# Optimization experiments

Measured on AMD Instinct MI355X. Metric: run time of the kernel, lower is better.

Reference implementation:

```python
import math
import jax, jax.numpy as jnp
import numpy as np
from jax.scipy.special import erf

D = 128                # cubic box / image size (even)
B, T = 4, 2            # particles, candidate poses per particle
GRID_DIST_DEGS = 8.0
GRID_STEP_DEGS = 2.0
PIXEL_SIZE = 1.5       # Angstrom / px
MAX_SHIFT_FRACTION = 0.2
TOP_K = 2
HALF_PARTICLE = 0.5 * D


def _rot_z(a):
    c, s = jnp.cos(a), jnp.sin(a)
    z, o = jnp.zeros_like(a), jnp.ones_like(a)
    return jnp.stack([jnp.stack([c, -s, z], -1),
                      jnp.stack([s, c, z], -1),
                      jnp.stack([z, z, o], -1)], -2)


def _rot_y(a):
    c, s = jnp.cos(a), jnp.sin(a)
    z, o = jnp.zeros_like(a), jnp.ones_like(a)
    return jnp.stack([jnp.stack([c, z, s], -1),
                      jnp.stack([z, o, z], -1),
                      jnp.stack([-s, z, c], -1)], -2)


def _euler_zyz_to_matrix(ang):
    # RELION convention ZYZ: R = Rz(a) @ Ry(b) @ Rz(c)
    return _rot_z(ang[..., 0]) @ _rot_y(ang[..., 1]) @ _rot_z(ang[..., 2])


def _so3_grid_rotmats():
    n = math.ceil(GRID_DIST_DEGS / GRID_STEP_DEGS)
    n = n if n % 2 == 1 else n + 1
    half = GRID_DIST_DEGS / 2.0
    a = np.linspace(-half, half, n)
    g = np.stack(np.meshgrid(a, a, a, indexing='ij'), -1).reshape(-1, 3)
    return _euler_zyz_to_matrix(jnp.deg2rad(jnp.asarray(g, jnp.float32)))


def _compute_dft(vol):
    # sinc^2 gridding pre-filter, then fftshifted rfftn of fftshifted volume
    d = vol.shape[-1]
    f = jnp.fft.fftshift(jnp.fft.fftfreq(d)).astype(vol.dtype)
    fz, fy, fx = jnp.meshgrid(f, f, f, indexing='ij')
    r = jnp.sqrt(fz * fz + fy * fy + fx * fx)
    vol = vol * jnp.sinc(r) ** 2
    dft = jnp.fft.rfftn(jnp.fft.fftshift(vol, axes=(-3, -2, -1)), axes=(-3, -2, -1))
    return jnp.fft.fftshift(dft, axes=(-3, -2))


def _trilinear_complex(vol, z, y, x):
    # trilinear interpolation into a complex 3D array, zero outside bounds
    Dz, Dy, Dx = vol.shape
    z0f, y0f, x0f = jnp.floor(z), jnp.floor(y), jnp.floor(x)
    fz, fy, fx = z - z0f, y - y0f, x - x0f
    z0, y0, x0 = z0f.astype(jnp.int32), y0f.astype(jnp.int32), x0f.astype(jnp.int32)

    def corner(zi, yi, xi, w):
        valid = (zi >= 0) & (zi < Dz) & (yi >= 0) & (yi < Dy) & (xi >= 0) & (xi < Dx)
        v = vol[jnp.clip(zi, 0, Dz - 1), jnp.clip(yi, 0, Dy - 1), jnp.clip(xi, 0, Dx - 1)]
        return jnp.where(valid, v * w, jnp.zeros((), vol.dtype))

    out = corner(z0, y0, x0, (1 - fz) * (1 - fy) * (1 - fx))
    out = out + corner(z0, y0, x0 + 1, (1 - fz) * (1 - fy) * fx)
    out = out + corner(z0, y0 + 1, x0, (1 - fz) * fy * (1 - fx))
    out = out + corner(z0, y0 + 1, x0 + 1, (1 - fz) * fy * fx)
    out = out + corner(z0 + 1, y0, x0, fz * (1 - fy) * (1 - fx))
    out = out + corner(z0 + 1, y0, x0 + 1, fz * (1 - fy) * fx)
    out = out + corner(z0 + 1, y0 + 1, x0, fz * fy * (1 - fx))
    out = out + corner(z0 + 1, y0 + 1, x0 + 1, fz * fy * fx)
    return out


def _extract_central_slices_rfft_3d(vol_rfft, d, rotmats):
    # rotated central-slice extraction from a fftshifted rfft 3D volume
    fy = jnp.fft.fftshift(jnp.fft.fftfreq(d)).astype(jnp.float32)
    fx = jnp.fft.rfftfreq(d).astype(jnp.float32)
    gy, gx = jnp.meshgrid(fy, fx, indexing='ij')            # (H, Wr)
    coords = jnp.stack([jnp.zeros_like(gy), gy, gx], -1)    # zyx, z=0 plane
    Rzyx = rotmats[..., ::-1, ::-1]                         # xyz rotmat -> zyx
    rot = jnp.einsum('...ij,hwj->...hwi', Rzyx, coords)     # (...,H,Wr,3)
    conj_mask = rot[..., 2] < 0                             # redundant half
    rot = jnp.where(conj_mask[..., None], -rot, rot)
    zi = rot[..., 0] * d + d // 2
    yi = rot[..., 1] * d + d // 2
    xi = rot[..., 2] * d
    s = _trilinear_complex(vol_rfft, zi, yi, xi)
    return jnp.where(conj_mask, jnp.conj(s), s)


def _forward(vol, imgs, ctf, rotmats, grid_rotmats):
    d = vol.shape[-1]
    vol_rfft = _compute_dft(vol)                            # (d, d, d//2+1)
    # _real_to_fourier
    fimg = jnp.fft.fftshift(
        jnp.fft.rfftn(jnp.fft.fftshift(imgs, axes=(-2, -1)), axes=(-2, -1)),
        axes=(-2,))                                         # (B, d, d//2+1)
    # compose pose candidates with the local SO3 grid: rotmats @ grid_rotmats
    exp_R = jnp.einsum('gjk,btij->btgik', grid_rotmats, rotmats)   # (B,T,G,3,3)
    projs = _extract_central_slices_rfft_3d(vol_rfft, d, exp_R)    # (B,T,G,H,Wr)
    projs = projs * ctf[:, None, None]
    # correlate_dft_2d
    prod = fimg[:, None, None] * jnp.conj(projs)
    prod = jnp.fft.ifftshift(prod, axes=(-2,))
    corrs = jnp.fft.ifftshift(jnp.fft.irfftn(prod, s=(d, d), axes=(-2, -1)),
                              axes=(-2, -1))                # (B,T,G,d,d) real
    # constrained peak search within max_shift_fraction window
    delta = math.ceil(d * (1.0 - MAX_SHIFT_FRACTION) / 2)
    h0 = delta
    c = corrs[..., h0:d - delta, h0:d - delta]
    maxJ = jnp.max(c, -1)
    argJ = jnp.argmax(c, -1)
    perImgCorr = jnp.max(maxJ, -1)                          # (B,T,G)
    argI = jnp.argmax(maxJ, -1)
    col = jnp.take_along_axis(argJ, argI[..., None], -1)[..., 0]
    shiftsXY = jnp.stack([h0 + col, h0 + argI], -1)         # (B,T,G,2) as (x,y)
    b = perImgCorr.shape[0]
    nrots = perImgCorr.shape[2]
    flat = perImgCorr.reshape(b, -1)                        # (B, T*G)
    maxCorrs, maxIdxs = jax.lax.top_k(flat, TOP_K)
    bestShifts = jnp.take_along_axis(shiftsXY.reshape(b, -1, 2),
                                     maxIdxs[..., None], axis=1)   # (B,K,2)
    mean = jnp.mean(flat, -1, keepdims=True)
    std = jnp.std(flat, -1, keepdims=True, ddof=1)
    comparedWeight = 0.5 * (1.0 + erf((maxCorrs - mean) / (std * 1.4142135623730951)))
    predShiftsAngs = -(bestShifts.astype(jnp.float32) - HALF_PARTICLE) * PIXEL_SIZE
    predRotMats = grid_rotmats[maxIdxs % nrots]             # (B,K,3,3)
    return maxCorrs, predRotMats, predShiftsAngs, comparedWeight


def setup_inputs() -> dict:
    key = jax.random.key(0)
    kv, ki, kc, kr = jax.random.split(key, 4)
    vol = jax.random.normal(kv, (D, D, D), jnp.float32)
    imgs = jax.random.normal(ki, (B, D, D), jnp.float32)
    ctf = jax.random.uniform(kc, (B, D, D // 2 + 1), jnp.float32, -1.0, 1.0)
    ang = jax.random.uniform(kr, (B, T, 3), jnp.float32, -np.pi, np.pi)
    rotmats = _euler_zyz_to_matrix(ang)
    grid_rotmats = _so3_grid_rotmats()
    return {"vol": vol, "imgs": imgs, "ctf": ctf, "rotmats": rotmats,
            "grid_rotmats": grid_rotmats}


def reference(vol, imgs, ctf, rotmats, grid_rotmats):
    return _forward(vol, imgs, ctf, rotmats, grid_rotmats)
```

## Files before the change

### kernel.cpp

```cpp
#include <hip/hip_runtime.h>
#include <hip/hip_fp16.h>
#include <math.h>
#include <float.h>

#define DD   128
#define KX   65
#define NB   4
#define NTT  2
#define NG   125
#define NBTG (NB*NTT*NG)
#define WIN  24
#define H0   52

#define QZ  132
#define QY  131
#define QX  68
#define QPLANE (QY*QX)
#define QN  (QZ*QY*QX)

typedef unsigned int u32;

__device__ __forceinline__ float2 cmul(float2 a, float2 b){
    return make_float2(a.x*b.x - a.y*b.y, a.x*b.y + a.y*b.x);
}

__device__ __forceinline__ void make_tw(float2* sTw, int tid){
    if (tid < 128){
        float s, c;
        sincosf((float)tid * (float)(M_PI/64.0), &s, &c);
        sTw[tid] = make_float2(c, s);
    }
}

__global__ __launch_bounds__(256) void k_stageA(const float* __restrict__ vol,
                       const float* __restrict__ imgs,
                       float2* __restrict__ A1, float2* __restrict__ B1){
    __shared__ float2 sZ [16*DD];
    __shared__ float2 sZ2[16*DD];
    __shared__ float2 sTw[128];
    int tid = threadIdx.x;
    int bid = blockIdx.x;
    make_tw(sTw, tid);
    __syncthreads();

    if (bid < 512){
        int z = bid >> 2, q = bid & 3;
        int y0 = q*32;
        float fz = (z-64)*(1.0f/128.0f);
        for (int i = tid; i < 16*DD; i += 256){
            int p = i >> 7, x = i & 127;
            int yA = y0 + 2*p;
            float fx = (x-64)*(1.0f/128.0f);
            float fyA = (yA-64)*(1.0f/128.0f);
            float fyB = fyA + (1.0f/128.0f);
            float b2 = fz*fz + fx*fx;
            float rA = sqrtf(b2 + fyA*fyA);
            float rB = sqrtf(b2 + fyB*fyB);
            float sA = (rA > 0.f) ? (sinf((float)M_PI*rA)/((float)M_PI*rA)) : 1.f;
            float sB = (rB > 0.f) ? (sinf((float)M_PI*rB)/((float)M_PI*rB)) : 1.f;
            float a = vol[(z*DD + yA)*DD + x] * sA * sA;
            float b = vol[(z*DD + yA+1)*DD + x] * sB * sB;
            sZ[i] = make_float2(a, b);
        }
        __syncthreads();
        for (int i = tid; i < 16*32; i += 256){
            int p = i >> 5, x1 = i & 31;
            int b0 = p*DD + x1;
            float2 a = sZ[b0], bb = sZ[b0+32], c2 = sZ[b0+64], d = sZ[b0+96];
            float acx=a.x+c2.x, acy=a.y+c2.y;
            float amx=a.x-c2.x, amy=a.y-c2.y;
            float bdx=bb.x+d.x, bdy=bb.y+d.y;
            float bmx=bb.x-d.x, bmy=bb.y-d.y;
            sZ[b0   ] = make_float2(acx+bdx, acy+bdy);
            sZ[b0+32] = make_float2(amx+bmy, amy-bmx);
            sZ[b0+64] = make_float2(acx-bdx, acy-bdy);
            sZ[b0+96] = make_float2(amx-bmy, amy+bmx);
        }
        __syncthreads();
        for (int i = tid; i < 16*32; i += 256){
            int p = i >> 5, r5 = i & 31;
            int c = r5 >> 3, x2 = r5 & 7;
            int b0 = p*DD + 32*c + x2;
            float2 u0 = sZ[b0], u1 = sZ[b0+8], u2 = sZ[b0+16], u3 = sZ[b0+24];
            float2 w1 = sTw[(8*c)&127];  w1.y = -w1.y;
            float2 w2 = sTw[(16*c)&127]; w2.y = -w2.y;
            float2 w3 = sTw[(24*c)&127]; w3.y = -w3.y;
            float2 t1 = cmul(u1,w1), t2 = cmul(u2,w2), t3 = cmul(u3,w3);
            float2 pp = make_float2(u0.x+t2.x, u0.y+t2.y);
            float2 qq = make_float2(u0.x-t2.x, u0.y-t2.y);
            float2 rr = make_float2(t1.x+t3.x, t1.y+t3.y);
            float2 ss = make_float2(t1.x-t3.x, t1.y-t3.y);
            sZ[b0   ] = make_float2(pp.x+rr.x, pp.y+rr.y);
            sZ[b0+8 ] = make_float2(qq.x+ss.y, qq.y-ss.x);
            sZ[b0+16] = make_float2(pp.x-rr.x, pp.y-rr.y);
            sZ[b0+24] = make_float2(qq.x-ss.y, qq.y+ss.x);
        }
        __syncthreads();
        for (int i = tid; i < 16*DD; i += 256){
            int p = i >> 7, k = i & 127;
            int c = k & 3, s = (k >> 2) & 3;
            const float2* v = &sZ[p*DD + 32*c + 8*s];
            float ar0=0,ai0=0,ar1=0,ai1=0;
            int j = 0;
            #pragma unroll
            for (int x2 = 0; x2 < 8; x2 += 2){
                float2 v0 = v[x2], v1 = v[x2+1];
                float2 e0 = sTw[j]; int jn = (j + k)&127;
                float2 e1 = sTw[jn];
                ar0 += v0.x*e0.x + v0.y*e0.y;  ai0 += v0.y*e0.x - v0.x*e0.y;
                ar1 += v1.x*e1.x + v1.y*e1.y;  ai1 += v1.y*e1.x - v1.x*e1.y;
                j = (jn + k)&127;
            }
            sZ2[i] = make_float2(ar0+ar1, ai0+ai1);
        }
        __syncthreads();
        for (int i = tid; i < 16*KX; i += 256){
            int p = i / KX, k = i - p*KX;
            float2 Zk = sZ2[p*DD + k];
            float2 Zm = sZ2[p*DD + ((128-k)&127)];
            float2 A = make_float2(0.5f*(Zk.x+Zm.x), 0.5f*(Zk.y-Zm.y));
            float Dx = Zk.x - Zm.x, Dy = Zk.y + Zm.y;
            float2 Bv = make_float2(0.5f*Dy, -0.5f*Dx);
            int yA = y0 + 2*p;
            A1[(z*DD + yA  )*KX + k] = A;
            A1[(z*DD + yA+1)*KX + k] = Bv;
        }
    } else {
        int o = (bid - 512)*256 + tid;
        if (o >= NB*DD*KX) return;
        int b = o / (DD*KX);
        int r = o - b*DD*KX;
        int y = r / KX, k = r - y*KX;
        const float* row = imgs + (b*DD + y)*DD;
        float ar0=0,ai0=0,ar1=0,ai1=0,ar2=0,ai2=0,ar3=0,ai3=0;
        int i0=0, i1=k&127, i2=(2*k)&127, i3=(3*k)&127;
        int st = (4*k)&127;
        for (int x = 0; x < DD; x += 4){
            float v0=row[x], v1=row[x+1], v2=row[x+2], v3=row[x+3];
            float2 e0=sTw[i0], e1=sTw[i1], e2=sTw[i2], e3=sTw[i3];
            ar0 += v0*e0.x; ai0 -= v0*e0.y;
            ar1 += v1*e1.x; ai1 -= v1*e1.y;
            ar2 += v2*e2.x; ai2 -= v2*e2.y;
            ar3 += v3*e3.x; ai3 -= v3*e3.y;
            i0=(i0+st)&127; i1=(i1+st)&127; i2=(i2+st)&127; i3=(i3+st)&127;
        }
        B1[o] = make_float2(ar0+ar1+ar2+ar3, ai0+ai1+ai2+ai3);
    }
}

__global__ __launch_bounds__(256) void k_stageB(const float2* __restrict__ A1,
                       const float* __restrict__ ctf, const float2* __restrict__ B1,
                       float2* __restrict__ A2, float2* __restrict__ Fc){
    __shared__ float2 sU[32*KX];
    __shared__ float2 sTw[128];
    int tid = threadIdx.x;
    int bid = blockIdx.x;
    make_tw(sTw, tid);
    __syncthreads();

    if (bid < 512){
        int z = bid >> 2, c = bid & 3;
        const float2* base = A1 + z*DD*KX;
        for (int i = tid; i < 32*KX; i += 256){
            int n = i / KX, kk = i - n*KX;
            float2 a  = base[(n    )*KX + kk];
            float2 bb = base[(n+32)*KX + kk];
            float2 c2 = base[(n+64)*KX + kk];
            float2 d  = base[(n+96)*KX + kk];
            float acx = a.x + c2.x, acy = a.y + c2.y;
            float amx = a.x - c2.x, amy = a.y - c2.y;
            float bdx = bb.x + d.x, bdy = bb.y + d.y;
            float bmx = bb.x - d.x, bmy = bb.y - d.y;
            float2 u;
            if (c == 0)      u = make_float2(acx + bdx, acy + bdy);
            else if (c == 2) u = make_float2(acx - bdx, acy - bdy);
            else if (c == 1) u = make_float2(amx + bmy, amy - bmx);
            else             u = make_float2(amx - bmy, amy + bmx);
            sU[i] = u;
        }
        __syncthreads();
        float2 w1 = sTw[(8*c)&127];  w1.y = -w1.y;
        float2 w2 = sTw[(16*c)&127]; w2.y = -w2.y;
        float2 w3 = sTw[(24*c)&127]; w3.y = -w3.y;
        for (int i = tid; i < 8*KX; i += 256){
            int n2 = i / KX, kk = i - n2*KX;
            int b0 = n2*KX + kk;
            float2 u0 = sU[b0], u1 = sU[b0+8*KX], u2 = sU[b0+16*KX], u3 = sU[b0+24*KX];
            float2 t1 = cmul(u1,w1), t2 = cmul(u2,w2), t3 = cmul(u3,w3);
            float2 p = make_float2(u0.x+t2.x, u0.y+t2.y);
            float2 q = make_float2(u0.x-t2.x, u0.y-t2.y);
            float2 r = make_float2(t1.x+t3.x, t1.y+t3.y);
            float2 s = make_float2(t1.x-t3.x, t1.y-t3.y);
            sU[b0       ] = make_float2(p.x+r.x, p.y+r.y);
            sU[b0+ 8*KX ] = make_float2(q.x+s.y, q.y-s.x);
            sU[b0+16*KX ] = make_float2(p.x-r.x, p.y-r.y);
            sU[b0+24*KX ] = make_float2(q.x-s.y, q.y+s.x);
        }
        __syncthreads();
        for (int o = tid; o < 32*KX; o += 256){
            int m = o / KX, kk = o - m*KX;
            int ky = 4*m + c;
            int s4 = m & 3;
            const float2* v = &sU[(8*s4)*KX + kk];
            float ar0=0,ai0=0,ar1=0,ai1=0;
            int j = 0;
            #pragma unroll
            for (int n2 = 0; n2 < 8; n2 += 2){
                float2 v0 = v[n2*KX], v1 = v[(n2+1)*KX];
                float2 e0 = sTw[j]; int jn = (j + ky)&127;
                float2 e1 = sTw[jn];
                ar0 += v0.x*e0.x + v0.y*e0.y;  ai0 += v0.y*e0.x - v0.x*e0.y;
                ar1 += v1.x*e1.x + v1.y*e1.y;  ai1 += v1.y*e1.x - v1.x*e1.y;
                j = (jn + ky)&127;
            }
            A2[(z*DD + ky)*KX + kk] = make_float2(ar0+ar1, ai0+ai1);
        }
    } else {
        int o = (bid - 512)*256 + tid;
        if (o >= NB*DD*KX) return;
        int b = o / (DD*KX);
        int r = o - b*DD*KX;
        int h = r / KX, k = r - h*KX;
        int kky = (h + 64) & 127;
        const float2* col = B1 + b*DD*KX + k;
        float ar0=0,ai0=0,ar1=0,ai1=0,ar2=0,ai2=0,ar3=0,ai3=0;
        int i0=0, i1=kky&127, i2=(2*kky)&127, i3=(3*kky)&127;
        int st = (4*kky)&127;
        for (int y = 0; y < DD; y += 4){
            float2 v0=col[(y+0)*KX], v1=col[(y+1)*KX];
            float2 v2=col[(y+2)*KX], v3=col[(y+3)*KX];
            float2 e0=sTw[i0], e1=sTw[i1], e2=sTw[i2], e3=sTw[i3];
            ar0 += v0.x*e0.x + v0.y*e0.y;  ai0 += v0.y*e0.x - v0.x*e0.y;
            ar1 += v1.x*e1.x + v1.y*e1.y;  ai1 += v1.y*e1.x - v1.x*e1.y;
            ar2 += v2.x*e2.x + v2.y*e2.y;  ai2 += v2.y*e2.x - v2.x*e2.y;
            ar3 += v3.x*e3.x + v3.y*e3.y;  ai3 += v3.y*e3.x - v3.x*e3.y;
            i0=(i0+st)&127; i1=(i1+st)&127; i2=(i2+st)&127; i3=(i3+st)&127;
        }
        float sgn = ((h + k)&1) ? -1.f : 1.f;
        float cf = ctf[o];
        Fc[o] = make_float2((ar0+ar1+ar2+ar3)*sgn*cf, (ai0+ai1+ai2+ai3)*sgn*cf);
    }
}

__global__ __launch_bounds__(256) void k_zero(uint4* __restrict__ p, int n4){
    int i = blockIdx.x*256 + threadIdx.x;
    for (; i < n4; i += 256*1024)
        p[i] = make_uint4(0,0,0,0);
}

__global__ __launch_bounds__(256) void k_volD(const float2* __restrict__ A2,
                       u32* __restrict__ Yh){
    __shared__ float2 sU[32*KX];
    __shared__ float2 sTw[128];
    int tid = threadIdx.x;
    int bid = blockIdx.x;
    int ky = bid >> 2, c = bid & 3;
    make_tw(sTw, tid);
    __syncthreads();

    const float2* base = A2 + ky*KX;
    for (int i = tid; i < 32*KX; i += 256){
        int n = i / KX, kk = i - n*KX;
        float2 a  = base[(n    )*DD*KX + kk];
        float2 bb = base[(n+32)*DD*KX + kk];
        float2 c2 = base[(n+64)*DD*KX + kk];
        float2 d  = base[(n+96)*DD*KX + kk];
        float acx = a.x + c2.x, acy = a.y + c2.y;
        float amx = a.x - c2.x, amy = a.y - c2.y;
        float bdx = bb.x + d.x, bdy = bb.y + d.y;
        float bmx = bb.x - d.x, bmy = bb.y - d.y;
        float2 u;
        if (c == 0)      u = make_float2(acx + bdx, acy + bdy);
        else if (c == 2) u = make_float2(acx - bdx, acy - bdy);
        else if (c == 1) u = make_float2(amx + bmy, amy - bmx);
        else             u = make_float2(amx - bmy, amy + bmx);
        sU[i] = u;
    }
    __syncthreads();
    float2 w1 = sTw[(8*c)&127];  w1.y = -w1.y;
    float2 w2 = sTw[(16*c)&127]; w2.y = -w2.y;
    float2 w3 = sTw[(24*c)&127]; w3.y = -w3.y;
    for (int i = tid; i < 8*KX; i += 256){
        int n2 = i / KX, kk = i - n2*KX;
        int b0 = n2*KX + kk;
        float2 u0 = sU[b0], u1 = sU[b0+8*KX], u2 = sU[b0+16*KX], u3 = sU[b0+24*KX];
        float2 t1 = cmul(u1,w1), t2 = cmul(u2,w2), t3 = cmul(u3,w3);
        float2 p = make_float2(u0.x+t2.x, u0.y+t2.y);
        float2 q = make_float2(u0.x-t2.x, u0.y-t2.y);
        float2 r = make_float2(t1.x+t3.x, t1.y+t3.y);
        float2 s = make_float2(t1.x-t3.x, t1.y-t3.y);
        sU[b0       ] = make_float2(p.x+r.x, p.y+r.y);
        sU[b0+ 8*KX ] = make_float2(q.x+s.y, q.y-s.x);
        sU[b0+16*KX ] = make_float2(p.x-r.x, p.y-r.y);
        sU[b0+24*KX ] = make_float2(q.x-s.y, q.y+s.x);
    }
    __syncthreads();
    int hy = (ky + 64) & 127;
    for (int o = tid; o < 32*KX; o += 256){
        int m = o / KX, kk = o - m*KX;
        int kz = 4*m + c;
        int hz = (kz + 64) & 127;
        int s4 = m & 3;
        const float2* v = &sU[(8*s4)*KX + kk];
        float ar0=0,ai0=0,ar1=0,ai1=0;
        int j = 0;
        #pragma unroll
        for (int n2 = 0; n2 < 8; n2 += 2){
            float2 v0 = v[n2*KX], v1 = v[(n2+1)*KX];
            float2 e0 = sTw[j]; int jn = (j + kz)&127;
            float2 e1 = sTw[jn];
            ar0 += v0.x*e0.x + v0.y*e0.y;  ai0 += v0.y*e0.x - v0.x*e0.y;
            ar1 += v1.x*e1.x + v1.y*e1.y;  ai1 += v1.y*e1.x - v1.x*e1.y;
            j = (jn + kz)&127;
        }
        float sgn = ((hz + hy + kk) & 1) ? -1.f : 1.f;
        __half2 hv = __floats2half2_rn((ar0+ar1)*sgn, (ai0+ai1)*sgn);
        u32 hp = *reinterpret_cast<u32*>(&hv);
        int z = hz + 1, y = hy + 1;
        Yh[2*((z*QY + y    )*QX + kk)    ] = hp;
        Yh[2*((z*QY + y - 1)*QX + kk) + 1] = hp;
    }
}

__device__ __forceinline__ float2 slice_point(const u32* __restrict__ Yh,
        float2 f, float xi, float zi, float yi){
    bool neg = xi < 0.f;
    if (neg){ xi = -xi; zi = 128.f - zi; yi = 128.f - yi; }
    xi = fminf(xi, 65.f);
    zi = fminf(fmaxf(zi, -1.f), 129.f);
    yi = fminf(fmaxf(yi, -1.f), 129.f);
    float zf = floorf(zi), yf = floorf(yi), xf = floorf(xi);
    float fz = zi - zf, fy = yi - yf, fx = xi - xf;
    int z0 = (int)zf, y0 = (int)yf, x0 = (int)xf;
    int qi = ((z0+1)*QY + (y0+1))*QX + x0;
    uint4 A = *reinterpret_cast<const uint4*>(Yh + 2*qi);
    uint4 B = *reinterpret_cast<const uint4*>(Yh + 2*(qi + QPLANE));
    float gx = 1.f - fx, gy = 1.f - fy, gz = 1.f - fz;
    float2 aL0 = __half22float2(*reinterpret_cast<const __half2*>(&A.x));
    float2 aH0 = __half22float2(*reinterpret_cast<const __half2*>(&A.y));
    float2 aL1 = __half22float2(*reinterpret_cast<const __half2*>(&A.z));
    float2 aH1 = __half22float2(*reinterpret_cast<const __half2*>(&A.w));
    float2 bL0 = __half22float2(*reinterpret_cast<const __half2*>(&B.x));
    float2 bH0 = __half22float2(*reinterpret_cast<const __half2*>(&B.y));
    float2 bL1 = __half22float2(*reinterpret_cast<const __half2*>(&B.z));
    float2 bH1 = __half22float2(*reinterpret_cast<const __half2*>(&B.w));
    float ar0 = aL0.x*gx + aL1.x*fx, ai0 = aL0.y*gx + aL1.y*fx;
    float ar1 = aH0.x*gx + aH1.x*fx, ai1 = aH0.y*gx + aH1.y*fx;
    float br0 = bL0.x*gx + bL1.x*fx, bi0 = bL0.y*gx + bL1.y*fx;
    float br1 = bH0.x*gx + bH1.x*fx, bi1 = bH0.y*gx + bH1.y*fx;
    float cr = ar0*gy + ar1*fy, ci = ai0*gy + ai1*fy;
    float dr = br0*gy + br1*fy, di = bi0*gy + bi1*fy;
    float sr = cr*gz + dr*fz,   si = ci*gz + di*fz;
    if (neg) si = -si;
    return make_float2(f.x*sr + f.y*si, f.y*sr - f.x*si);
}

__global__ __launch_bounds__(256,5) void k_main(
    const u32* __restrict__ Yh, const float2* __restrict__ Fc,
    const float* __restrict__ rotm, const float* __restrict__ grid,
    float* __restrict__ resVal, int2* __restrict__ resShift)
{
    __shared__ float2 sP[DD*16];
    __shared__ float2 sT[WIN*KX];
    __shared__ float2 sTw[128];
    __shared__ float  sM[9];
    __shared__ float  swv[4];
    __shared__ int    swi[4];

    int tid = threadIdx.x;
    int nb  = blockIdx.x;
    int blk = (nb & 7)*125 + (nb >> 3);
    int b  = blk / (NTT*NG);
    int rr = blk - b*NTT*NG;
    int t  = rr / NG;
    int g  = rr - t*NG;

    make_tw(sTw, tid);
    if (tid < 9){
        int i = tid/3, k = tid - 3*i;
        const float* R  = rotm + (b*NTT + t)*9;
        const float* Gm = grid + g*9;
        sM[tid] = R[i*3+0]*Gm[0*3+k] + R[i*3+1]*Gm[1*3+k] + R[i*3+2]*Gm[2*3+k];
    }
    __syncthreads();

    float M00=sM[0], M01=sM[1], M10=sM[3], M11=sM[4], M20=sM[6], M21=sM[7];
    const float2* FcB = Fc + b*DD*KX;

    if (tid < 128){
        int h = tid;
        float hf = (float)(h - 64);
        float xi = M01*hf + M00*64.f;
        float zi = M21*hf + M20*64.f + 64.f;
        float yi = M11*hf + M10*64.f + 64.f;
        sP[h] = slice_point(Yh, FcB[h*KX + 64], xi, zi, yi);
    }
    __syncthreads();
    if (tid < 96){
        int a = tid >> 2, p = tid & 3;
        int ry = (116 + a) & 127;
        int idx = (32*p*ry) & 127;
        float ar = 0.f, ai = 0.f;
        const float2* v = &sP[32*p];
        #pragma unroll 8
        for (int h2 = 0; h2 < 32; ++h2){
            float2 e = sTw[idx];
            float2 pv = v[h2];
            ar += pv.x*e.x - pv.y*e.y;
            ai += pv.x*e.y + pv.y*e.x;
            idx = (idx + ry) & 127;
        }
        sP[256 + tid] = make_float2(ar, ai);
    }
    __syncthreads();
    if (tid < 24){
        float2 p0 = sP[256 + tid*4 + 0];
        float2 p1 = sP[256 + tid*4 + 1];
        float2 p2 = sP[256 + tid*4 + 2];
        float2 p3 = sP[256 + tid*4 + 3];
        float sg = (tid & 1) ? -(1.f/128.f) : (1.f/128.f);
        sT[tid*KX + 64] = make_float2((p0.x+p1.x+p2.x+p3.x)*sg,
                                      (p0.y+p1.y+p2.y+p3.y)*sg);
    }
    __syncthreads();

    const int kk = tid & 15;
    const int h0 = tid >> 4;
    const float hf0 = (float)(h0 - 64);
    const float dxi = 16.f*M01, dzi = 16.f*M21, dyi = 16.f*M11;

    for (int cc = 0; cc < 4; ++cc){
        int w = cc*16 + kk;
        float wf = (float)w;
        float xi0 = M01*hf0 + M00*wf;
        float zi0 = M21*hf0 + M20*wf + 64.f;
        float yi0 = M11*hf0 + M10*wf + 64.f;
        int fidx = h0*KX + w;

        #pragma unroll 2
        for (int j = 0; j < 8; ++j){
            sP[tid + 256*j] = slice_point(Yh, FcB[fidx], xi0, zi0, yi0);
            xi0 += dxi; zi0 += dzi; yi0 += dyi; fidx += 16*KX;
        }
        __syncthreads();

        #pragma unroll
        for (int rep = 0; rep < 2; ++rep){
            int i = tid + 256*rep;
            float2 a  = sP[i];
            float2 bb = sP[i + 512];
            float2 c2 = sP[i + 1024];
            float2 d  = sP[i + 1536];
            float acx = a.x + c2.x, acy = a.y + c2.y;
            float amx = a.x - c2.x, amy = a.y - c2.y;
            float bdx = bb.x + d.x, bdy = bb.y + d.y;
            float bmx = bb.x - d.x, bmy = bb.y - d.y;
            sP[i       ] = make_float2(acx + bdx, acy + bdy);
            sP[i + 512 ] = make_float2(amx - bmy, amy + bmx);
            sP[i + 1024] = make_float2(acx - bdx, acy - bdy);
            sP[i + 1536] = make_float2(amx + bmy, amy - bmx);
        }
        __syncthreads();

        #pragma unroll
        for (int rep = 0; rep < 2; ++rep){
            int i = tid + 256*rep;
            int c = i >> 7, r7 = i & 127;
            int b0 = (c << 9) + r7;
            float2 u0 = sP[b0], u1 = sP[b0+128], u2 = sP[b0+256], u3 = sP[b0+384];
            float2 w1 = sTw[(8*c)&127], w2 = sTw[(16*c)&127], w3 = sTw[(24*c)&127];
            float2 t1 = cmul(u1,w1), t2 = cmul(u2,w2), t3 = cmul(u3,w3);
            float2 p  = make_float2(u0.x+t2.x, u0.y+t2.y);
            float2 qq = make_float2(u0.x-t2.x, u0.y-t2.y);
            float2 r  = make_float2(t1.x+t3.x, t1.y+t3.y);
            float2 s  = make_float2(t1.x-t3.x, t1.y-t3.y);
            sP[b0      ] = make_float2(p.x+r.x,  p.y+r.y);
            sP[b0 + 128] = make_float2(qq.x-s.y, qq.y+s.x);
            sP[b0 + 256] = make_float2(p.x-r.x,  p.y-r.y);
            sP[b0 + 384] = make_float2(qq.x+s.y, qq.y-s.x);
        }
        __syncthreads();

        for (int o = tid; o < 24*16; o += 256){
            int a = o >> 4, kx = o & 15;
            int ry = (116 + a) & 127;
            int c = ry & 3, s4 = (ry >> 2) & 3;
            const float2* v = &sP[(c << 9) + (s4 << 7) + kx];
            float ar0=0,ai0=0,ar1=0,ai1=0;
            int j2 = 0;
            #pragma unroll
            for (int n2 = 0; n2 < 8; n2 += 2){
                float2 v0 = v[n2*16], v1 = v[(n2+1)*16];
                float2 e0 = sTw[j2]; int jn = (j2 + ry)&127;
                float2 e1 = sTw[jn];
                ar0 += v0.x*e0.x - v0.y*e0.y;  ai0 += v0.x*e0.y + v0.y*e0.x;
                ar1 += v1.x*e1.x - v1.y*e1.y;  ai1 += v1.x*e1.y + v1.y*e1.x;
                j2 = (jn + ry)&127;
            }
            float sg = (a & 1) ? -(1.f/128.f) : (1.f/128.f);
            sT[a*KX + cc*16 + kx] = make_float2((ar0+ar1)*sg, (ai0+ai1)*sg);
        }
        __syncthreads();
    }

    float2* sPf = sP;
    for (int o = tid; o < WIN*31; o += 256){
        int a = o / 31, km1 = o - a*31;
        int k = km1 + 1;
        const float2* Trow = &sT[a*KX];
        float2 T1 = Trow[k], T2 = Trow[64-k];
        sPf[a*31 + km1]       = make_float2(T1.x + T2.x, T1.y - T2.y);
        sPf[744 + a*31 + km1] = make_float2(T1.x - T2.x, T1.y + T2.y);
    }
    __syncthreads();

    float* sC = reinterpret_cast<float*>(sP + 1488);
    for (int o = tid; o < WIN*WIN; o += 256){
        int a = o / WIN, bx = o - a*WIN;
        int rx = (116 + bx) & 127;
        const float2* Trow = &sT[a*KX];
        float2 T32 = Trow[32];
        float base = Trow[0].x + ((bx & 1) ? -Trow[64].x : Trow[64].x);
        int r4 = rx & 3;
        base += (r4==0) ?  2.f*T32.x : (r4==1) ? -2.f*T32.y
              : (r4==2) ? -2.f*T32.x :  2.f*T32.y;
        const float2* A = sPf + ((bx & 1) ? 744 : 0) + a*31 - 1;
        float acc0 = 0.f, acc1 = 0.f;
        int j1 = rx, j2 = (2*rx)&127;
        int st = (2*rx)&127;
        for (int k = 1; k < 31; k += 2){
            float2 e1 = sTw[j1]; float2 A1v = A[k];
            float2 e2 = sTw[j2]; float2 A2v = A[k+1];
            acc0 += A1v.x*e1.x - A1v.y*e1.y;
            acc1 += A2v.x*e2.x - A2v.y*e2.y;
            j1=(j1+st)&127; j2=(j2+st)&127;
        }
        {
            float2 e = sTw[(31*rx)&127]; float2 Av = A[31];
            acc0 += Av.x*e.x - Av.y*e.y;
        }
        sC[o] = (base + 2.f*(acc0+acc1))*(1.f/128.f);
    }
    __syncthreads();

    float best = -FLT_MAX; int bidx = 0x7fffffff;
    for (int i = tid; i < WIN*WIN; i += 256){
        float v = sC[i];
        if (v > best){ best = v; bidx = i; }
    }
    #pragma unroll
    for (int s = 32; s > 0; s >>= 1){
        float ov = __shfl_xor(best, s, 64);
        int   oi = __shfl_xor(bidx, s, 64);
        if (ov > best || (ov == best && oi < bidx)){ best = ov; bidx = oi; }
    }
    if ((tid & 63) == 0){ swv[tid>>6] = best; swi[tid>>6] = bidx; }
    __syncthreads();
    if (tid == 0){
        float bv = swv[0]; int bi = swi[0];
        #pragma unroll
        for (int w2 = 1; w2 < 4; ++w2){
            if (swv[w2] > bv || (swv[w2] == bv && swi[w2] < bi)){ bv = swv[w2]; bi = swi[w2]; }
        }
        int a = bi / WIN, bx = bi - a*WIN;
        resVal[blk] = bv;
        resShift[blk] = make_int2(H0 + bx, H0 + a);
    }
}

__global__ __launch_bounds__(256) void k_final(const float* __restrict__ resVal,
                        const int2* __restrict__ resShift,
                        const float* __restrict__ grid, float* __restrict__ out)
{
    __shared__ float sv[256];
    __shared__ int   si[256];
    __shared__ float sr[256];
    __shared__ float sMean;
    const int N = NTT*NG;
    int b = blockIdx.x, tid = threadIdx.x;
    const float* v = resVal + b*N;
    float myv = (tid < N) ? v[tid] : -FLT_MAX;

    sv[tid] = myv; si[tid] = (tid < N) ? tid : 0x7fffffff;
    __syncthreads();
    for (int s = 128; s > 0; s >>= 1){
        if (tid < s){
            float v2 = sv[tid+s]; int i2 = si[tid+s];
            if (v2 > sv[tid] || (v2 == sv[tid] && i2 < si[tid])){ sv[tid]=v2; si[tid]=i2; }
        }
        __syncthreads();
    }
    float v0 = sv[0]; int i0 = si[0];
    __syncthreads();

    bool act = (tid < N) && (tid != i0);
    sv[tid] = act ? myv : -FLT_MAX; si[tid] = act ? tid : 0x7fffffff;
    __syncthreads();
    for (int s = 128; s > 0; s >>= 1){
        if (tid < s){
            float v2 = sv[tid+s]; int i2 = si[tid+s];
            if (v2 > sv[tid] || (v2 == sv[tid] && i2 < si[tid])){ sv[tid]=v2; si[tid]=i2; }
        }
        __syncthreads();
    }
    float v1 = sv[0]; int i1 = si[0];
    __syncthreads();

    sr[tid] = (tid < N) ? myv : 0.f;
    __syncthreads();
    for (int s = 128; s > 0; s >>= 1){
        if (tid < s) sr[tid] += sr[tid+s];
        __syncthreads();
    }
    if (tid == 0) sMean = sr[0] / (float)N;
    __syncthreads();
    float mean = sMean;

    float d = (tid < N) ? (myv - mean) : 0.f;
    sr[tid] = d*d;
    __syncthreads();
    for (int s = 128; s > 0; s >>= 1){
        if (tid < s) sr[tid] += sr[tid+s];
        __syncthreads();
    }

    if (tid == 0){
        float stdv = sqrtf(sr[0] / (float)(N - 1));
        float vals[2] = {v0, v1};
        int   idxs[2] = {i0, i1};
        for (int k = 0; k < 2; ++k){
            out[b*2 + k] = vals[k];
            int gi = idxs[k] % NG;
            for (int j = 0; j < 9; ++j) out[8 + (b*2+k)*9 + j] = grid[gi*9 + j];
            int2 sh = resShift[b*N + idxs[k]];
            out[80 + (b*2+k)*2 + 0] = -((float)sh.x - 64.f)*1.5f;
            out[80 + (b*2+k)*2 + 1] = -((float)sh.y - 64.f)*1.5f;
            out[96 + b*2 + k] = 0.5f*(1.f + erff((vals[k] - mean)/(stdv*1.41421356237309515f)));
        }
    }
}

extern "C" void kernel_launch(void* const* d_in, const int* in_sizes, int n_in,
                              void* d_out, int out_size, void* d_ws, size_t ws_size,
                              hipStream_t stream)
{
    const float* vol  = (const float*)d_in[0];
    const float* imgs = (const float*)d_in[1];
    const float* ctf  = (const float*)d_in[2];
    const float* rotm = (const float*)d_in[3];
    const float* grid = (const float*)d_in[4];
    float* out = (float*)d_out;

    const size_t A1_BYTES  = (size_t)DD*DD*KX*sizeof(float2);
    const size_t B1_BYTES  = (size_t)NB*DD*KX*sizeof(float2);
    const size_t YH_BYTES  = (size_t)QN*8;

    char* ws = (char*)d_ws;
    float2* A1 = (float2*)(ws);
    float2* B1 = (float2*)(ws + A1_BYTES);
    u32*    Yh = (u32*)(ws);
    size_t off = YH_BYTES;
    float2* A2 = (float2*)(ws + off); off += A1_BYTES;
    float2* Fc = (float2*)(ws + off); off += B1_BYTES;
    float* resVal = (float*)(ws + off); off += (size_t)NBTG*sizeof(float);
    int2* resShift = (int2*)(ws + off); off += (size_t)NBTG*sizeof(int2);

    const int n4 = (int)(YH_BYTES / 16);
    k_stageA<<<642, 256, 0, stream>>>(vol, imgs, A1, B1);
    k_stageB<<<642, 256, 0, stream>>>(A1, ctf, B1, A2, Fc);
    k_zero  <<<1024,256, 0, stream>>>((uint4*)Yh, n4);
    k_volD  <<<512, 256, 0, stream>>>(A2, Yh);
    k_main  <<<NBTG,256, 0, stream>>>(Yh, Fc, rotm, grid, resVal, resShift);
    k_final <<<NB,  256, 0, stream>>>(resVal, resShift, grid, out);
}
```

Before: 109.2 us.

## Fuse Yh zeroing into stage A and batch gather loads in main slice loop

```diff
diff --git a/kernel.cpp b/kernel.cpp
--- a/kernel.cpp
+++ b/kernel.cpp
@@ -34,12 +34,20 @@
 
 __global__ __launch_bounds__(256) void k_stageA(const float* __restrict__ vol,
                        const float* __restrict__ imgs,
-                       float2* __restrict__ A1, float2* __restrict__ B1){
+                       float2* __restrict__ A1, float2* __restrict__ B1,
+                       uint4* __restrict__ Yz, int n4){
     __shared__ float2 sZ [16*DD];
     __shared__ float2 sZ2[16*DD];
     __shared__ float2 sTw[128];
     int tid = threadIdx.x;
     int bid = blockIdx.x;
+
+    if (bid >= 642){
+        int i = (bid - 642)*256 + tid;
+        for (; i < n4; i += 256*256)
+            Yz[i] = make_uint4(0,0,0,0);
+        return;
+    }
     make_tw(sTw, tid);
     __syncthreads();
 
@@ -242,12 +250,6 @@
     }
 }
 
-__global__ __launch_bounds__(256) void k_zero(uint4* __restrict__ p, int n4){
-    int i = blockIdx.x*256 + threadIdx.x;
-    for (; i < n4; i += 256*1024)
-        p[i] = make_uint4(0,0,0,0);
-}
-
 __global__ __launch_bounds__(256) void k_volD(const float2* __restrict__ A2,
                        u32* __restrict__ Yh){
     __shared__ float2 sU[32*KX];
@@ -322,20 +324,23 @@
     }
 }
 
-__device__ __forceinline__ float2 slice_point(const u32* __restrict__ Yh,
-        float2 f, float xi, float zi, float yi){
+struct GP { int qi; float fx, fy, fz; bool neg; };
+
+__device__ __forceinline__ GP gp_coords(float xi, float zi, float yi){
+    GP g;
     bool neg = xi < 0.f;
     if (neg){ xi = -xi; zi = 128.f - zi; yi = 128.f - yi; }
     xi = fminf(xi, 65.f);
     zi = fminf(fmaxf(zi, -1.f), 129.f);
     yi = fminf(fmaxf(yi, -1.f), 129.f);
     float zf = floorf(zi), yf = floorf(yi), xf = floorf(xi);
-    float fz = zi - zf, fy = yi - yf, fx = xi - xf;
-    int z0 = (int)zf, y0 = (int)yf, x0 = (int)xf;
-    int qi = ((z0+1)*QY + (y0+1))*QX + x0;
-    uint4 A = *reinterpret_cast<const uint4*>(Yh + 2*qi);
-    uint4 B = *reinterpret_cast<const uint4*>(Yh + 2*(qi + QPLANE));
-    float gx = 1.f - fx, gy = 1.f - fy, gz = 1.f - fz;
+    g.fz = zi - zf; g.fy = yi - yf; g.fx = xi - xf; g.neg = neg;
+    g.qi = (((int)zf + 1)*QY + ((int)yf + 1))*QX + (int)xf;
+    return g;
+}
+
+__device__ __forceinline__ float2 gp_eval(uint4 A, uint4 B, GP g, float2 f){
+    float gx = 1.f - g.fx, gy = 1.f - g.fy, gz = 1.f - g.fz;
     float2 aL0 = __half22float2(*reinterpret_cast<const __half2*>(&A.x));
     float2 aH0 = __half22float2(*reinterpret_cast<const __half2*>(&A.y));
     float2 aL1 = __half22float2(*reinterpret_cast<const __half2*>(&A.z));
@@ -344,18 +349,18 @@
     float2 bH0 = __half22float2(*reinterpret_cast<const __half2*>(&B.y));
     float2 bL1 = __half22float2(*reinterpret_cast<const __half2*>(&B.z));
     float2 bH1 = __half22float2(*reinterpret_cast<const __half2*>(&B.w));
-    float ar0 = aL0.x*gx + aL1.x*fx, ai0 = aL0.y*gx + aL1.y*fx;
-    float ar1 = aH0.x*gx + aH1.x*fx, ai1 = aH0.y*gx + aH1.y*fx;
-    float br0 = bL0.x*gx + bL1.x*fx, bi0 = bL0.y*gx + bL1.y*fx;
-    float br1 = bH0.x*gx + bH1.x*fx, bi1 = bH0.y*gx + bH1.y*fx;
-    float cr = ar0*gy + ar1*fy, ci = ai0*gy + ai1*fy;
-    float dr = br0*gy + br1*fy, di = bi0*gy + bi1*fy;
-    float sr = cr*gz + dr*fz,   si = ci*gz + di*fz;
-    if (neg) si = -si;
+    float ar0 = aL0.x*gx + aL1.x*g.fx, ai0 = aL0.y*gx + aL1.y*g.fx;
+    float ar1 = aH0.x*gx + aH1.x*g.fx, ai1 = aH0.y*gx + aH1.y*g.fx;
+    float br0 = bL0.x*gx + bL1.x*g.fx, bi0 = bL0.y*gx + bL1.y*g.fx;
+    float br1 = bH0.x*gx + bH1.x*g.fx, bi1 = bH0.y*gx + bH1.y*g.fx;
+    float cr = ar0*gy + ar1*g.fy, ci = ai0*gy + ai1*g.fy;
+    float dr = br0*gy + br1*g.fy, di = bi0*gy + bi1*g.fy;
+    float sr = cr*gz + dr*g.fz,   si = ci*gz + di*g.fz;
+    if (g.neg) si = -si;
     return make_float2(f.x*sr + f.y*si, f.y*sr - f.x*si);
 }
 
-__global__ __launch_bounds__(256,5) void k_main(
+__global__ __launch_bounds__(256,4) void k_main(
     const u32* __restrict__ Yh, const float2* __restrict__ Fc,
     const float* __restrict__ rotm, const float* __restrict__ grid,
     float* __restrict__ resVal, int2* __restrict__ resShift)
@@ -393,7 +398,10 @@
         float xi = M01*hf + M00*64.f;
         float zi = M21*hf + M20*64.f + 64.f;
         float yi = M11*hf + M10*64.f + 64.f;
-        sP[h] = slice_point(Yh, FcB[h*KX + 64], xi, zi, yi);
+        GP g0 = gp_coords(xi, zi, yi);
+        uint4 A = *reinterpret_cast<const uint4*>(Yh + 2*g0.qi);
+        uint4 B = *reinterpret_cast<const uint4*>(Yh + 2*(g0.qi + QPLANE));
+        sP[h] = gp_eval(A, B, g0, FcB[h*KX + 64]);
     }
     __syncthreads();
     if (tid < 96){
@@ -437,10 +445,34 @@
         float yi0 = M11*hf0 + M10*wf + 64.f;
         int fidx = h0*KX + w;
 
-        #pragma unroll 2
-        for (int j = 0; j < 8; ++j){
-            sP[tid + 256*j] = slice_point(Yh, FcB[fidx], xi0, zi0, yi0);
+        #pragma unroll
+        for (int jb = 0; jb < 2; ++jb){
+            GP g0 = gp_coords(xi0, zi0, yi0);
+            float2 f0 = FcB[fidx];
             xi0 += dxi; zi0 += dzi; yi0 += dyi; fidx += 16*KX;
+            GP g1 = gp_coords(xi0, zi0, yi0);
+            float2 f1 = FcB[fidx];
+            xi0 += dxi; zi0 += dzi; yi0 += dyi; fidx += 16*KX;
+            GP g2 = gp_coords(xi0, zi0, yi0);
+            float2 f2 = FcB[fidx];
+            xi0 += dxi; zi0 += dzi; yi0 += dyi; fidx += 16*KX;
+            GP g3 = gp_coords(xi0, zi0, yi0);
+            float2 f3 = FcB[fidx];
+            xi0 += dxi; zi0 += dzi; yi0 += dyi; fidx += 16*KX;
+
+            uint4 A0 = *reinterpret_cast<const uint4*>(Yh + 2*g0.qi);
+            uint4 B0 = *reinterpret_cast<const uint4*>(Yh + 2*(g0.qi + QPLANE));
+            uint4 A1v = *reinterpret_cast<const uint4*>(Yh + 2*g1.qi);
+            uint4 B1v = *reinterpret_cast<const uint4*>(Yh + 2*(g1.qi + QPLANE));
+            uint4 A2v = *reinterpret_cast<const uint4*>(Yh + 2*g2.qi);
+            uint4 B2v = *reinterpret_cast<const uint4*>(Yh + 2*(g2.qi + QPLANE));
+            uint4 A3v = *reinterpret_cast<const uint4*>(Yh + 2*g3.qi);
+            uint4 B3v = *reinterpret_cast<const uint4*>(Yh + 2*(g3.qi + QPLANE));
+
+            sP[tid + 256*(4*jb+0)] = gp_eval(A0,  B0,  g0, f0);
+            sP[tid + 256*(4*jb+1)] = gp_eval(A1v, B1v, g1, f1);
+            sP[tid + 256*(4*jb+2)] = gp_eval(A2v, B2v, g2, f2);
+            sP[tid + 256*(4*jb+3)] = gp_eval(A3v, B3v, g3, f3);
         }
         __syncthreads();
 
@@ -651,24 +683,23 @@
     const float* grid = (const float*)d_in[4];
     float* out = (float*)d_out;
 
+    const size_t YH_BYTES  = (size_t)QN*8;
     const size_t A1_BYTES  = (size_t)DD*DD*KX*sizeof(float2);
     const size_t B1_BYTES  = (size_t)NB*DD*KX*sizeof(float2);
-    const size_t YH_BYTES  = (size_t)QN*8;
 
     char* ws = (char*)d_ws;
-    float2* A1 = (float2*)(ws);
-    float2* B1 = (float2*)(ws + A1_BYTES);
     u32*    Yh = (u32*)(ws);
     size_t off = YH_BYTES;
+    float2* A1 = (float2*)(ws + off); off += A1_BYTES;
+    float2* B1 = (float2*)(ws + off); off += B1_BYTES;
     float2* A2 = (float2*)(ws + off); off += A1_BYTES;
     float2* Fc = (float2*)(ws + off); off += B1_BYTES;
     float* resVal = (float*)(ws + off); off += (size_t)NBTG*sizeof(float);
     int2* resShift = (int2*)(ws + off); off += (size_t)NBTG*sizeof(int2);
 
     const int n4 = (int)(YH_BYTES / 16);
-    k_stageA<<<642, 256, 0, stream>>>(vol, imgs, A1, B1);
+    k_stageA<<<898, 256, 0, stream>>>(vol, imgs, A1, B1, (uint4*)Yh, n4);
     k_stageB<<<642, 256, 0, stream>>>(A1, ctf, B1, A2, Fc);
-    k_zero  <<<1024,256, 0, stream>>>((uint4*)Yh, n4);
     k_volD  <<<512, 256, 0, stream>>>(A2, Yh);
     k_main  <<<NBTG,256, 0, stream>>>(Yh, Fc, rotm, grid, resVal, resShift);
     k_final <<<NB,  256, 0, stream>>>(resVal, resShift, grid, out);
```

Result: faster. 103.2 us (-5.6%).
